# Kernel optimization log

Measured on AMD Instinct MI355X. Metric: run time of the kernel, lower is better.

Reference implementation:

```python
import jax, jax.numpy as jnp
import numpy as np

B, S, D, H, MEM, P = 32, 512, 768, 8, 768, 3
DK = D // H
LN_EPS = 1e-6


def _layer_norm(x, a, b):
    # torch LayerNorm in source uses unbiased std (ddof=1) and adds eps to std
    mean = x.mean(-1, keepdims=True)
    var = ((x - mean) ** 2).sum(-1, keepdims=True) / (x.shape[-1] - 1)
    return a * (x - mean) / (jnp.sqrt(var) + LN_EPS) + b


def _gcn_branch(x, mask, Wq, bq, Wk, bk, Ws, bs):
    # x: [B,S,D], mask: [B,S] 0/1 ints
    q = (x @ Wq.T + bq).reshape(B, S, H, DK).transpose(0, 2, 1, 3)  # [B,H,S,DK]
    k = (x @ Wk.T + bk).reshape(B, S, H, DK).transpose(0, 2, 1, 3)
    scores = jnp.einsum('bhqd,bhkd->bhqk', q, k) / jnp.sqrt(jnp.float32(DK))
    scores = jnp.where(mask[:, None, None, :] == 0, jnp.float32(-1e9), scores)
    adj = jax.nn.softmax(scores, axis=-1).mean(1)  # average heads -> [B,S,S]
    # adj - diag(diag(adj)) + I  ==  set diagonal to 1
    idx = jnp.arange(S)
    adj = adj.at[:, idx, idx].set(1.0)
    adj = adj * mask[:, :, None].astype(adj.dtype)  # src_mask.transpose(1,2) * adj
    denom = adj.sum(-1, keepdims=True) + 1.0
    out = x
    for W, b in zip(Ws, bs):
        out = jax.nn.relu((adj @ out @ W.T + b) / denom)
    return out, adj


def _proj(a, b):
    # Proj(a, b): (a.b / |b|) * normalize(b)
    b_mo = jnp.sqrt((b * b).sum(-1))
    axb = (a * b).sum(-1)
    bn = b / jnp.maximum(jnp.sqrt((b * b).sum(-1, keepdims=True)), 1e-12)
    return (axb / b_mo)[:, None] * bn


def setup_inputs() -> dict:
    key = jax.random.key(0)
    ks = jax.random.split(key, 32)

    def w(k, shape):
        return jax.random.normal(k, shape, jnp.float32) * 0.02

    inp = {
        'sequence_output': jax.random.normal(ks[0], (B, S, D), jnp.float32),
        'pooled_output': jax.random.normal(ks[1], (B, D), jnp.float32),
        'src_mask': jnp.ones((B, S), jnp.int32),
        'aspect_mask': jnp.ones((B, S), jnp.float32),
        'ln_a': jnp.ones((D,), jnp.float32),
        'ln_b': jnp.zeros((D,), jnp.float32),
        'fp_Wq': w(ks[2], (D, D)), 'fp_bq': jnp.zeros((D,), jnp.float32),
        'fp_Wk': w(ks[3], (D, D)), 'fp_bk': jnp.zeros((D,), jnp.float32),
        'fp_W0': w(ks[4], (MEM, D)), 'fp_b0': jnp.zeros((MEM,), jnp.float32),
        'fp_W1': w(ks[5], (MEM, MEM)), 'fp_b1': jnp.zeros((MEM,), jnp.float32),
        'fc_Wq': w(ks[6], (D, D)), 'fc_bq': jnp.zeros((D,), jnp.float32),
        'fc_Wk': w(ks[7], (D, D)), 'fc_bk': jnp.zeros((D,), jnp.float32),
        'fc_W0': w(ks[8], (MEM, D)), 'fc_b0': jnp.zeros((MEM,), jnp.float32),
        'fc_W1': w(ks[9], (MEM, MEM)), 'fc_b1': jnp.zeros((MEM,), jnp.float32),
        'fp_dense_W': w(ks[10], (P, MEM)), 'fp_dense_b': jnp.zeros((P,), jnp.float32),
        'fc_dense_W': w(ks[11], (P, MEM)), 'fc_dense_b': jnp.zeros((P,), jnp.float32),
    }
    return inp


def reference(sequence_output, pooled_output, src_mask, aspect_mask,
              ln_a, ln_b,
              fp_Wq, fp_bq, fp_Wk, fp_bk, fp_W0, fp_b0, fp_W1, fp_b1,
              fc_Wq, fc_bq, fc_Wk, fc_bk, fc_W0, fc_b0, fc_W1, fc_b1,
              fp_dense_W, fp_dense_b, fc_dense_W, fc_dense_b):
    label_embedding = pooled_output
    att_inputs = _layer_norm(sequence_output, ln_a, ln_b)  # dropout disabled (eval)
    asp_wn = aspect_mask.sum(1)[:, None]  # [B,1]

    fp_out, _ = _gcn_branch(att_inputs, src_mask, fp_Wq, fp_bq, fp_Wk, fp_bk,
                            [fp_W0, fp_W1], [fp_b0, fp_b1])
    fc_out, _ = _gcn_branch(att_inputs, src_mask, fc_Wq, fc_bq, fc_Wk, fc_bk,
                            [fc_W0, fc_W1], [fc_b0, fc_b1])

    outputs_fp = fp_out.sum(1)  # [B,MEM]
    outputs_fc = (fc_out * aspect_mask[:, :, None]).sum(1) / asp_wn  # [B,MEM]

    fp_x = _proj(outputs_fp, outputs_fc)
    fp_y = _proj(outputs_fp, outputs_fp - fp_x)
    fc_y = outputs_fc  # gradient-reverse layer is identity in forward

    logits_p = fp_y @ fp_dense_W.T + fp_dense_b
    logits_c = fc_y @ fc_dense_W.T + fc_dense_b
    return (logits_p, logits_c, fp_y, label_embedding)
```

## Files before the change

### kernel.cpp

```cpp
#include <hip/hip_runtime.h>
#include <math.h>
#include <stdint.h>

#define Bn 32
#define Sn 512
#define Dn 768
#define Hn 8
#define DKn 96
#define Pn 3

typedef __bf16 bf16_t;
typedef bf16_t bf16x8 __attribute__((ext_vector_type(8)));
typedef float f32x4 __attribute__((ext_vector_type(4)));

__device__ __forceinline__ bf16_t f2bf(float f) { return (bf16_t)f; }

__device__ __forceinline__ void gload16(const void* g, void* l) {
    __builtin_amdgcn_global_load_lds((const __attribute__((address_space(1))) void*)g,
                                     (__attribute__((address_space(3))) void*)l, 16, 0, 0);
}

__device__ __forceinline__ float brsum(float v, float* red) {
    int t = threadIdx.x;
    red[t] = v; __syncthreads();
    #pragma unroll
    for (int o = 128; o > 0; o >>= 1) {
        if (t < o) red[t] += red[t + o];
        __syncthreads();
    }
    float r = red[0]; __syncthreads();
    return r;
}

__global__ __launch_bounds__(256) void ln_kernel(const float* __restrict__ in,
                                                 const float* __restrict__ ga,
                                                 const float* __restrict__ gb,
                                                 bf16_t* __restrict__ out) {
    __shared__ float red[256];
    long row = blockIdx.x;
    const float* x = in + row * Dn;
    bf16_t* y = out + row * Dn;
    int t = threadIdx.x;
    float v0 = x[t], v1 = x[t + 256], v2 = x[t + 512];
    float mean = brsum(v0 + v1 + v2, red) / (float)Dn;
    float d0 = v0 - mean, d1 = v1 - mean, d2 = v2 - mean;
    float ss = brsum(d0 * d0 + d1 * d1 + d2 * d2, red);
    float inv = 1.0f / (sqrtf(ss / (float)(Dn - 1)) + 1e-6f);
    y[t]       = f2bf(ga[t]       * d0 * inv + gb[t]);
    y[t + 256] = f2bf(ga[t + 256] * d1 * inv + gb[t + 256]);
    y[t + 512] = f2bf(ga[t + 512] * d2 * inv + gb[t + 512]);
}

__global__ __launch_bounds__(256) void cvt8(const float* __restrict__ s0,
                                            const float* __restrict__ s1,
                                            const float* __restrict__ s2,
                                            const float* __restrict__ s3,
                                            const float* __restrict__ s4,
                                            const float* __restrict__ s5,
                                            const float* __restrict__ s6,
                                            const float* __restrict__ s7,
                                            bf16_t* __restrict__ dst) {
    int y = blockIdx.y;
    const float* s = (y == 0) ? s0 : (y == 1) ? s1 : (y == 2) ? s2 : (y == 3) ? s3
                   : (y == 4) ? s4 : (y == 5) ? s5 : (y == 6) ? s6 : s7;
    long i = (long)blockIdx.x * 1024 + threadIdx.x * 4;
    float4 v = *reinterpret_cast<const float4*>(s + i);
    bf16_t* d = dst + (long)y * Dn * Dn + i;
    d[0] = f2bf(v.x); d[1] = f2bf(v.y); d[2] = f2bf(v.z); d[3] = f2bf(v.w);
}

__global__ __launch_bounds__(256) void biascat_k(const float* __restrict__ s0,
                                                 const float* __restrict__ s1,
                                                 const float* __restrict__ s2,
                                                 const float* __restrict__ s3,
                                                 const float* __restrict__ s4,
                                                 const float* __restrict__ s5,
                                                 const float* __restrict__ s6,
                                                 const float* __restrict__ s7,
                                                 float* __restrict__ dst) {
    int y = blockIdx.x;
    const float* s = (y == 0) ? s0 : (y == 1) ? s1 : (y == 2) ? s2 : (y == 3) ? s3
                   : (y == 4) ? s4 : (y == 5) ? s5 : (y == 6) ? s6 : s7;
    for (int i = threadIdx.x; i < Dn; i += 256) dst[(long)y * Dn + i] = s[i];
}

__global__ void zero_kernel(float* p, int n) {
    int i = blockIdx.x * 256 + threadIdx.x;
    if (i < n) p[i] = 0.0f;
}

template <int EPI>
__global__ __launch_bounds__(512, 1) void gemm256(
    const bf16_t* __restrict__ Ag, const bf16_t* __restrict__ Bg,
    bf16_t* __restrict__ Cg, float* __restrict__ outv,
    int lda, int ldb, int ldc, int K,
    long sAhi, long sAlo, long sBhi, long sBlo, long sChi, long sClo,
    int lgZ,
    const float* __restrict__ bias, long bias_zs,
    const float* __restrict__ denom,
    const float* __restrict__ aspw) {
    __shared__ __align__(16) bf16_t lds[4][2][8192];

    unsigned gx = gridDim.x, gy = gridDim.y;
    unsigned nwg = gx * gy * gridDim.z;
    unsigned flat = (blockIdx.z * gy + blockIdx.y) * gx + blockIdx.x;
    unsigned q8 = nwg >> 3, r8 = nwg & 7;
    unsigned xcd = flat & 7, idx = flat >> 3;
    unsigned swz = (xcd < r8 ? xcd * (q8 + 1) : r8 * (q8 + 1) + (xcd - r8) * q8) + idx;
    unsigned bx = swz % gx;
    unsigned rest = swz / gx;
    unsigned by = rest % gy;
    unsigned zz = rest / gy;
    int zb = zz >> lgZ;
    int zg = zz & ((1 << lgZ) - 1);
    long zful = zz;

    const bf16_t* A = Ag + zb * sAhi + zg * sAlo;
    const bf16_t* B = Bg + zb * sBhi + zg * sBlo;

    int n0 = bx * 256, m0 = by * 256;
    int tid = threadIdx.x;
    int lane = tid & 63, w = tid >> 6;
    int wm = w >> 2, wn = w & 3;

    const int NT = K >> 5;

    int srow = lane & 15;
    int skc = (lane >> 4) * 8;
    const bf16_t* Asrc0 = A + (size_t)(m0 + (w * 2 + 0) * 16 + srow) * lda + skc;
    const bf16_t* Asrc1 = A + (size_t)(m0 + (w * 2 + 1) * 16 + srow) * lda + skc;
    const bf16_t* Bsrc0 = B + (size_t)(n0 + (w * 2 + 0) * 16 + srow) * ldb + skc;
    const bf16_t* Bsrc1 = B + (size_t)(n0 + (w * 2 + 1) * 16 + srow) * ldb + skc;
    int c0off = (w * 2 + 0) * 512 + lane * 8;
    int c1off = (w * 2 + 1) * 512 + lane * 8;

    f32x4 acc[8][4];
    #pragma unroll
    for (int i = 0; i < 8; ++i)
        #pragma unroll
        for (int j = 0; j < 4; ++j) acc[i][j] = (f32x4){0.f, 0.f, 0.f, 0.f};

    #pragma unroll
    for (int tt = 0; tt < 3; ++tt) {
        gload16(Asrc0 + tt * 32, &lds[tt][0][c0off]);
        gload16(Asrc1 + tt * 32, &lds[tt][0][c1off]);
        gload16(Bsrc0 + tt * 32, &lds[tt][1][c0off]);
        gload16(Bsrc1 + tt * 32, &lds[tt][1][c1off]);
    }
    asm volatile("s_waitcnt vmcnt(8)" ::: "memory");
    __builtin_amdgcn_s_barrier();

    int aoff = wm * 8 * 512 + lane * 8;
    int boff = wn * 4 * 512 + lane * 8;

    for (int t = 0; t < NT; ++t) {
        const bf16_t* bufA = &lds[t & 3][0][0];
        const bf16_t* bufB = &lds[t & 3][1][0];
        int tn = t + 3;
        bf16_t* dA = &lds[tn & 3][0][0];
        bf16_t* dB = &lds[tn & 3][1][0];
        bool st = tn < NT;

        bf16x8 a[4], b[4];
        #pragma unroll
        for (int i = 0; i < 4; ++i)
            a[i] = *(const bf16x8*)(bufA + aoff + i * 512);
        #pragma unroll
        for (int j = 0; j < 4; ++j)
            b[j] = *(const bf16x8*)(bufB + boff + j * 512);
        if (st) {
            gload16(Asrc0 + tn * 32, dA + c0off);
            gload16(Bsrc0 + tn * 32, dB + c0off);
        }
        __builtin_amdgcn_s_barrier();
        asm volatile("s_waitcnt lgkmcnt(0)" ::: "memory");
        __builtin_amdgcn_sched_barrier(0);
        __builtin_amdgcn_s_setprio(1);
        #pragma unroll
        for (int i = 0; i < 4; ++i)
            #pragma unroll
            for (int j = 0; j < 4; ++j)
                acc[i][j] = __builtin_amdgcn_mfma_f32_16x16x32_bf16(a[i], b[j], acc[i][j], 0, 0, 0);
        __builtin_amdgcn_s_setprio(0);
        __builtin_amdgcn_s_barrier();

        #pragma unroll
        for (int i = 0; i < 4; ++i)
            a[i] = *(const bf16x8*)(bufA + aoff + (4 + i) * 512);
        if (st) {
            gload16(Asrc1 + tn * 32, dA + c1off);
            gload16(Bsrc1 + tn * 32, dB + c1off);
        }
        __builtin_amdgcn_s_barrier();
        asm volatile("s_waitcnt lgkmcnt(0)" ::: "memory");
        __builtin_amdgcn_sched_barrier(0);
        __builtin_amdgcn_s_setprio(1);
        #pragma unroll
        for (int i = 0; i < 4; ++i)
            #pragma unroll
            for (int j = 0; j < 4; ++j)
                acc[4 + i][j] = __builtin_amdgcn_mfma_f32_16x16x32_bf16(a[i], b[j], acc[4 + i][j], 0, 0, 0);
        __builtin_amdgcn_s_setprio(0);
        if (t + 3 < NT)      asm volatile("s_waitcnt vmcnt(8)" ::: "memory");
        else if (t + 2 < NT) asm volatile("s_waitcnt vmcnt(4)" ::: "memory");
        else                 asm volatile("s_waitcnt vmcnt(0)" ::: "memory");
        __builtin_amdgcn_s_barrier();
    }

    int nb = n0 + wn * 64 + (lane & 15);
    int mbase = m0 + wm * 128 + (lane >> 4) * 4;
    const float* bz = bias ? bias + zb * bias_zs : nullptr;

    if (EPI == 0) {
        bf16_t* Cz = Cg + zb * sChi + zg * sClo;
        #pragma unroll
        for (int i = 0; i < 8; ++i) {
            #pragma unroll
            for (int r = 0; r < 4; ++r) {
                long m = mbase + i * 16 + r;
                bf16_t* crow = Cz + m * (long)ldc;
                #pragma unroll
                for (int j = 0; j < 4; ++j) {
                    int col = nb + j * 16;
                    float v = acc[i][j][r];
                    if (bz) v += bz[col];
                    crow[col] = f2bf(v);
                }
            }
        }
    } else if (EPI == 1) {
        bf16_t* Cz = Cg + zb * sChi + zg * sClo;
        const float* dz = denom + zful * Sn;
        #pragma unroll
        for (int i = 0; i < 8; ++i) {
            #pragma unroll
            for (int r = 0; r < 4; ++r) {
                int m = mbase + i * 16 + r;
                float dinv = 1.0f / dz[m];
                bf16_t* crow = Cz + (long)m * ldc;
                #pragma unroll
                for (int j = 0; j < 4; ++j) {
                    float v = fmaxf((acc[i][j][r] + bz[nb + j * 16]) * dinv, 0.0f);
                    crow[nb + j * 16] = f2bf(v);
                }
            }
        }
    } else {
        const float* dz = denom + zful * Sn;
        float csum[4] = {0.f, 0.f, 0.f, 0.f};
        #pragma unroll
        for (int i = 0; i < 8; ++i) {
            #pragma unroll
            for (int r = 0; r < 4; ++r) {
                int m = mbase + i * 16 + r;
                float dinv = 1.0f / dz[m];
                float wgt = (aspw && zb) ? aspw[(long)zg * Sn + m] : 1.0f;
                #pragma unroll
                for (int j = 0; j < 4; ++j) {
                    float v = fmaxf((acc[i][j][r] + bz[nb + j * 16]) * dinv, 0.0f);
                    csum[j] += v * wgt;
                }
            }
        }
        #pragma unroll
        for (int j = 0; j < 4; ++j) {
            float s = csum[j];
            s += __shfl_xor(s, 16);
            s += __shfl_xor(s, 32);
            if (lane < 16) atomicAdd(&outv[zful * Dn + nb + j * 16], s);
        }
    }
}

__global__ __launch_bounds__(256) void fused_adj(
    const bf16_t* __restrict__ QK, bf16_t* __restrict__ adjb,
    float* __restrict__ denomv, const int* __restrict__ mask) {
    __shared__ __align__(16) bf16_t Ks[2][128 * 104];
    __shared__ float red[4][16];

    int L = blockIdx.x;
    int swzi = (L & 7) * 128 + (L >> 3);
    int brc = swzi >> 9;
    int rem = swzi & 511;
    int b = rem >> 4;
    int q0 = (rem & 15) * 32;

    int tid = threadIdx.x;
    int lane = tid & 63, w = tid >> 6;
    int mt = w >> 1, nh = w & 1;
    int g = lane >> 4, c = lane & 15;

    const int LDQ = 3072;
    const bf16_t* Qrow  = QK + ((long)b * Sn + q0 + mt * 16 + c) * LDQ + brc * 1536;
    const bf16_t* Kbase = QK + (long)b * Sn * LDQ + brc * 1536 + Dn;

    const int* mrow = mask + (long)b * Sn;
    unsigned mbits = 0;
    #pragma unroll
    for (int t = 0; t < 4; ++t)
        #pragma unroll
        for (int nj = 0; nj < 4; ++nj)
            if (mrow[t * 128 + nh * 64 + nj * 16 + c] != 0) mbits |= 1u << (t * 4 + nj);

    int srow[6], scc[6];
    #pragma unroll
    for (int p = 0; p < 6; ++p) { int gr = tid + p * 256; srow[p] = gr / 12; scc[p] = gr % 12; }

    f32x4 adjacc[4][4];
    #pragma unroll
    for (int t = 0; t < 4; ++t)
        #pragma unroll
        for (int nj = 0; nj < 4; ++nj) adjacc[t][nj] = (f32x4){0.f, 0.f, 0.f, 0.f};

    f32x4 S[4][4];
    bf16x8 kr0[6], kr1[6], aq[3], aqn[3];
    const float sal = 0.102062072615966f;

    #pragma unroll
    for (int p = 0; p < 6; ++p)
        kr0[p] = *(const bf16x8*)(Kbase + (long)srow[p] * LDQ + scc[p] * 8);
    #pragma unroll
    for (int ks = 0; ks < 3; ++ks)
        aq[ks] = *(const bf16x8*)(Qrow + ks * 32 + g * 8);
    #pragma unroll
    for (int p = 0; p < 6; ++p)
        *(bf16x8*)(&Ks[0][srow[p] * 104 + scc[p] * 8]) = kr0[p];
    #pragma unroll
    for (int p = 0; p < 6; ++p)
        kr1[p] = *(const bf16x8*)(Kbase + (long)(128 + srow[p]) * LDQ + scc[p] * 8);
    __syncthreads();

    for (int h = 0; h < Hn; ++h) {
        #pragma unroll
        for (int t = 0; t < 4; ++t)
            #pragma unroll
            for (int nj = 0; nj < 4; ++nj) S[t][nj] = (f32x4){0.f, 0.f, 0.f, 0.f};

        float rs[4];
        #pragma unroll
        for (int t = 0; t < 4; ++t) {
            int it = h * 4 + t;
            if (it + 2 < 32) {
                int nt = it + 2;
                const bf16_t* kp = Kbase + (long)((nt & 3) * 128) * LDQ + (nt >> 2) * 96;
                if ((t & 1) == 0) {
                    #pragma unroll
                    for (int p = 0; p < 6; ++p)
                        kr0[p] = *(const bf16x8*)(kp + (long)srow[p] * LDQ + scc[p] * 8);
                } else {
                    #pragma unroll
                    for (int p = 0; p < 6; ++p)
                        kr1[p] = *(const bf16x8*)(kp + (long)srow[p] * LDQ + scc[p] * 8);
                }
            }
            if (t == 2 && h < 7) {
                #pragma unroll
                for (int ks = 0; ks < 3; ++ks)
                    aqn[ks] = *(const bf16x8*)(Qrow + (h + 1) * 96 + ks * 32 + g * 8);
            }
            #pragma unroll
            for (int nj = 0; nj < 4; ++nj) {
                #pragma unroll
                for (int ks = 0; ks < 3; ++ks) {
                    bf16x8 bk = *(const bf16x8*)(&Ks[t & 1][(nh * 64 + nj * 16 + c) * 104 + ks * 32 + g * 8]);
                    S[t][nj] = __builtin_amdgcn_mfma_f32_16x16x32_bf16(aq[ks], bk, S[t][nj], 0, 0, 0);
                }
            }
            if (t == 3) {
                rs[0] = rs[1] = rs[2] = rs[3] = 0.f;
                #pragma unroll
                for (int tt = 0; tt < 4; ++tt)
                    #pragma unroll
                    for (int nj = 0; nj < 4; ++nj) {
                        float mkf = ((mbits >> (tt * 4 + nj)) & 1u) ? 1.0f : 0.0f;
                        #pragma unroll
                        for (int ri = 0; ri < 4; ++ri) {
                            float e = mkf * __expf(S[tt][nj][ri] * sal);
                            S[tt][nj][ri] = e;
                            rs[ri] += e;
                        }
                    }
                #pragma unroll
                for (int ri = 0; ri < 4; ++ri) {
                    rs[ri] += __shfl_xor(rs[ri], 1);
                    rs[ri] += __shfl_xor(rs[ri], 2);
                    rs[ri] += __shfl_xor(rs[ri], 4);
                    rs[ri] += __shfl_xor(rs[ri], 8);
                }
                if (c == 0) {
                    #pragma unroll
                    for (int ri = 0; ri < 4; ++ri) red[w][g * 4 + ri] = rs[ri];
                }
            }
            if (it + 1 < 32) {
                if ((t & 1) == 0) {
                    #pragma unroll
                    for (int p = 0; p < 6; ++p)
                        *(bf16x8*)(&Ks[1][srow[p] * 104 + scc[p] * 8]) = kr1[p];
                } else {
                    #pragma unroll
                    for (int p = 0; p < 6; ++p)
                        *(bf16x8*)(&Ks[0][srow[p] * 104 + scc[p] * 8]) = kr0[p];
                }
            }
            __syncthreads();
            if (t == 3) {
                float inv[4];
                #pragma unroll
                for (int ri = 0; ri < 4; ++ri)
                    inv[ri] = 0.125f / (red[w][g * 4 + ri] + red[w ^ 1][g * 4 + ri]);
                #pragma unroll
                for (int tt = 0; tt < 4; ++tt)
                    #pragma unroll
                    for (int nj = 0; nj < 4; ++nj)
                        #pragma unroll
                        for (int ri = 0; ri < 4; ++ri)
                            adjacc[tt][nj][ri] += S[tt][nj][ri] * inv[ri];
                if (h < 7) {
                    #pragma unroll
                    for (int ks = 0; ks < 3; ++ks) aq[ks] = aqn[ks];
                }
            }
        }
    }

    float rm[4];
    #pragma unroll
    for (int ri = 0; ri < 4; ++ri)
        rm[ri] = (mrow[q0 + mt * 16 + g * 4 + ri] != 0) ? 1.0f : 0.0f;
    float rs2[4] = {0.f, 0.f, 0.f, 0.f};
    #pragma unroll
    for (int t = 0; t < 4; ++t)
        #pragma unroll
        for (int nj = 0; nj < 4; ++nj) {
            int n = t * 128 + nh * 64 + nj * 16 + c;
            #pragma unroll
            for (int ri = 0; ri < 4; ++ri) {
                float v = adjacc[t][nj][ri];
                int q = q0 + mt * 16 + g * 4 + ri;
                if (n == q) v = 1.0f;
                v *= rm[ri];
                adjacc[t][nj][ri] = v;
                rs2[ri] += v;
            }
        }
    #pragma unroll
    for (int ri = 0; ri < 4; ++ri) {
        rs2[ri] += __shfl_xor(rs2[ri], 1);
        rs2[ri] += __shfl_xor(rs2[ri], 2);
        rs2[ri] += __shfl_xor(rs2[ri], 4);
        rs2[ri] += __shfl_xor(rs2[ri], 8);
    }
    __syncthreads();
    if (c == 0) {
        #pragma unroll
        for (int ri = 0; ri < 4; ++ri) red[w][g * 4 + ri] = rs2[ri];
    }
    __syncthreads();
    long zful = (long)brc * Bn + b;
    if (nh == 0 && c == 0) {
        #pragma unroll
        for (int ri = 0; ri < 4; ++ri)
            denomv[zful * Sn + q0 + mt * 16 + g * 4 + ri] =
                red[w][g * 4 + ri] + red[w ^ 1][g * 4 + ri] + 1.0f;
    }
    bf16_t* stg = &Ks[0][0];
    #pragma unroll
    for (int t = 0; t < 4; ++t)
        #pragma unroll
        for (int nj = 0; nj < 4; ++nj) {
            int n = t * 128 + nh * 64 + nj * 16 + c;
            #pragma unroll
            for (int ri = 0; ri < 4; ++ri)
                stg[(mt * 16 + g * 4 + ri) * 520 + n] = f2bf(adjacc[t][nj][ri]);
        }
    __syncthreads();
    bf16_t* arow = adjb + (zful * Sn + q0) * Sn;
    #pragma unroll
    for (int p = 0; p < 8; ++p) {
        int gr = tid + p * 256;
        int row = gr >> 6, cc = gr & 63;
        *(bf16x8*)(arow + (long)row * Sn + cc * 8) = *(const bf16x8*)(stg + row * 520 + cc * 8);
    }
}

__global__ __launch_bounds__(256) void final_kernel(const float* __restrict__ ofp,
                                                    const float* __restrict__ ofc_raw,
                                                    const float* __restrict__ aspect,
                                                    const float* __restrict__ pooled,
                                                    const float* __restrict__ fpdW,
                                                    const float* __restrict__ fpdb,
                                                    const float* __restrict__ fcdW,
                                                    const float* __restrict__ fcdb,
                                                    float* __restrict__ out) {
    __shared__ float red[256];
    __shared__ float fp[Dn], fc[Dn], fy[Dn];
    int b = blockIdx.x, t = threadIdx.x;
    float awv = aspect[(long)b * Sn + t] + aspect[(long)b * Sn + t + 256];
    float asp_wn = brsum(awv, red);
    for (int i = t; i < Dn; i += 256) {
        fp[i] = ofp[(long)b * Dn + i];
        fc[i] = ofc_raw[(long)b * Dn + i] / asp_wn;
    }
    __syncthreads();
    float p0 = 0.0f, p1 = 0.0f;
    for (int i = t; i < Dn; i += 256) { p0 += fc[i] * fc[i]; p1 += fp[i] * fc[i]; }
    float dfc2 = brsum(p0, red);
    float dfpfc = brsum(p1, red);
    float bmo = sqrtf(dfc2);
    float coef = dfpfc / bmo;
    float bden = fmaxf(bmo, 1e-12f);
    float q0 = 0.0f, q1 = 0.0f;
    for (int i = t; i < Dn; i += 256) {
        float tv = fp[i] - coef * fc[i] / bden;
        fy[i] = tv;
        q0 += tv * tv;
        q1 += fp[i] * tv;
    }
    float dt2 = brsum(q0, red);
    float dfpt = brsum(q1, red);
    float tmo = sqrtf(dt2);
    float coef2 = dfpt / tmo;
    float tden = fmaxf(tmo, 1e-12f);
    for (int i = t; i < Dn; i += 256) fy[i] = coef2 * fy[i] / tden;
    __syncthreads();
    for (int i = t; i < Dn; i += 256) out[2 * Bn * Pn + (long)b * Dn + i] = fy[i];
    for (int i = t; i < Dn; i += 256)
        out[2 * Bn * Pn + Bn * Dn + (long)b * Dn + i] = pooled[(long)b * Dn + i];
    for (int j = 0; j < Pn; j++) {
        float lp = 0.0f, lc = 0.0f;
        for (int i = t; i < Dn; i += 256) {
            lp += fy[i] * fpdW[(long)j * Dn + i];
            lc += fc[i] * fcdW[(long)j * Dn + i];
        }
        float rp = brsum(lp, red);
        float rc = brsum(lc, red);
        if (t == 0) {
            out[(long)b * Pn + j] = rp + fpdb[j];
            out[Bn * Pn + (long)b * Pn + j] = rc + fcdb[j];
        }
    }
}

extern "C" void kernel_launch(void* const* d_in, const int* in_sizes, int n_in,
                              void* d_out, int out_size, void* d_ws, size_t ws_size,
                              hipStream_t stream) {
    const float* seq     = (const float*)d_in[0];
    const float* pooled  = (const float*)d_in[1];
    const int*   src_msk = (const int*)d_in[2];
    const float* aspect  = (const float*)d_in[3];
    const float* ln_a    = (const float*)d_in[4];
    const float* ln_b    = (const float*)d_in[5];
    float* out = (float*)d_out;

    const long NTD = (long)Bn * Sn * Dn;
    const long NSS = (long)Bn * Sn * Sn;
    const long DD  = (long)Dn * Dn;
    const long SD  = (long)Sn * Dn;

    char* w = (char*)d_ws;
    bf16_t* xbf   = (bf16_t*)w;
    bf16_t* QK    = xbf + NTD;
    bf16_t* H1    = QK;
    bf16_t* XT    = QK + 2 * NTD;
    bf16_t* adjb  = QK + 4 * NTD;
    float*  denom = (float*)(adjb + 2 * NSS);
    float*  ofp   = denom + 2L * Bn * Sn;
    float*  bcat  = ofp + 2L * Bn * Dn;
    bf16_t* Wb    = (bf16_t*)(bcat + 8 * Dn);

    ln_kernel<<<dim3(Bn * Sn), dim3(256), 0, stream>>>(seq, ln_a, ln_b, xbf);
    zero_kernel<<<dim3((2 * Bn * Dn + 255) / 256), dim3(256), 0, stream>>>(ofp, 2 * Bn * Dn);

    cvt8<<<dim3(576, 8), dim3(256), 0, stream>>>(
        (const float*)d_in[6], (const float*)d_in[8],
        (const float*)d_in[14], (const float*)d_in[16],
        (const float*)d_in[10], (const float*)d_in[18],
        (const float*)d_in[12], (const float*)d_in[20], Wb);
    biascat_k<<<dim3(8), dim3(256), 0, stream>>>(
        (const float*)d_in[7], (const float*)d_in[9],
        (const float*)d_in[15], (const float*)d_in[17],
        (const float*)d_in[11], (const float*)d_in[19],
        (const float*)d_in[13], (const float*)d_in[21], bcat);

    gemm256<0><<<dim3(12, 64, 1), dim3(512), 0, stream>>>(
        xbf, Wb, QK, nullptr, Dn, Dn, 3072, Dn,
        0, 0, 0, 0, 0, 0, 0, bcat, 0, nullptr, nullptr);

    fused_adj<<<dim3(2 * Bn * Sn / 32), dim3(256), 0, stream>>>(QK, adjb, denom, src_msk);

    gemm256<0><<<dim3(2, 3, 64), dim3(512), 0, stream>>>(
        Wb + 4 * DD, xbf, XT, nullptr, Dn, Dn, Sn, Dn,
        DD, 0, 0, SD, 32 * SD, SD,
        5, nullptr, 0, nullptr, nullptr);

    gemm256<1><<<dim3(3, 2, 64), dim3(512), 0, stream>>>(
        adjb, XT, H1, nullptr, Sn, Sn, Dn, Sn,
        32L * Sn * Sn, (long)Sn * Sn, 32 * SD, SD, 32 * SD, SD,
        5, bcat + 4 * Dn, Dn, denom, nullptr);

    gemm256<0><<<dim3(2, 3, 64), dim3(512), 0, stream>>>(
        Wb + 6 * DD, H1, XT, nullptr, Dn, Dn, Sn, Dn,
        DD, 0, 32 * SD, SD, 32 * SD, SD,
        5, nullptr, 0, nullptr, nullptr);

    gemm256<2><<<dim3(3, 2, 64), dim3(512), 0, stream>>>(
        adjb, XT, nullptr, ofp, Sn, Sn, 0, Sn,
        32L * Sn * Sn, (long)Sn * Sn, 32 * SD, SD, 0, 0,
        5, bcat + 6 * Dn, Dn, denom, aspect);

    final_kernel<<<dim3(Bn), dim3(256), 0, stream>>>(
        ofp, ofp + (long)Bn * Dn, aspect, pooled,
        (const float*)d_in[22], (const float*)d_in[23],
        (const float*)d_in[24], (const float*)d_in[25], out);
}
```

Measured before the change: 513.9 us.

## Add simple 128x128 GEMM for batched GCN stages and drop LDS staging in fused_adj

Adds a new 128x128-tile, 256-thread GEMM kernel (single-buffered LDS, direct global-to-LDS loads) and uses it for the four batched GCN GEMMs in place of the 256x256 tile kernel. This gives more workgroups and more occupancy, at the cost of less data reuse per tile and no software pipelining. fused_adj now reads K fragments straight from global memory into registers, double-buffered in registers, instead of staging them through shared memory. This removes most of its barriers, and it now declares 2 blocks per CU. The 256x256 kernel keeps only its EPI 0 path, which the QK projection still uses.

```diff
diff --git a/kernel.cpp b/kernel.cpp
--- a/kernel.cpp
+++ b/kernel.cpp
@@ -90,16 +90,17 @@
 }
 
 template <int EPI>
-__global__ __launch_bounds__(512, 1) void gemm256(
+__global__ __launch_bounds__(256) void gemm_bt(
     const bf16_t* __restrict__ Ag, const bf16_t* __restrict__ Bg,
     bf16_t* __restrict__ Cg, float* __restrict__ outv,
     int lda, int ldb, int ldc, int K,
     long sAhi, long sAlo, long sBhi, long sBlo, long sChi, long sClo,
-    int lgZ,
+    int lgZ, float alpha,
     const float* __restrict__ bias, long bias_zs,
     const float* __restrict__ denom,
     const float* __restrict__ aspw) {
-    __shared__ __align__(16) bf16_t lds[4][2][8192];
+    __shared__ __align__(16) bf16_t As[128 * 32];
+    __shared__ __align__(16) bf16_t Bs[128 * 32];
 
     unsigned gx = gridDim.x, gy = gridDim.y;
     unsigned nwg = gx * gy * gridDim.z;
@@ -118,6 +119,145 @@
     const bf16_t* A = Ag + zb * sAhi + zg * sAlo;
     const bf16_t* B = Bg + zb * sBhi + zg * sBlo;
 
+    int n0 = bx * 128;
+    int m0 = by * 128;
+    int tid = threadIdx.x;
+    int lane = tid & 63, wv = tid >> 6;
+    int wm = wv >> 1, wn = wv & 1;
+
+    int sub = lane >> 2;
+    int kcol = (lane & 3) * 8;
+    const bf16_t* pA0 = A + (size_t)(m0 + wv * 16 + sub) * lda + kcol;
+    const bf16_t* pA1 = pA0 + (size_t)64 * lda;
+    const bf16_t* pB0 = B + (size_t)(n0 + wv * 16 + sub) * ldb + kcol;
+    const bf16_t* pB1 = pB0 + (size_t)64 * ldb;
+    bf16_t* lA0 = As + wv * 512 + lane * 8;
+    bf16_t* lA1 = As + (4 + wv) * 512 + lane * 8;
+    bf16_t* lB0 = Bs + wv * 512 + lane * 8;
+    bf16_t* lB1 = Bs + (4 + wv) * 512 + lane * 8;
+
+    f32x4 acc[4][4];
+    #pragma unroll
+    for (int i = 0; i < 4; i++)
+        #pragma unroll
+        for (int j = 0; j < 4; j++) acc[i][j] = (f32x4){0.f, 0.f, 0.f, 0.f};
+
+    const bf16_t* ar = As + (wm * 64 + (lane & 15)) * 32 + (lane >> 4) * 8;
+    const bf16_t* br = Bs + (wn * 64 + (lane & 15)) * 32 + (lane >> 4) * 8;
+
+    for (int k0 = 0; k0 < K; k0 += 32) {
+        gload16(pA0 + k0, lA0);
+        gload16(pA1 + k0, lA1);
+        gload16(pB0 + k0, lB0);
+        gload16(pB1 + k0, lB1);
+        __syncthreads();
+        bf16x8 a[4], b[4];
+        #pragma unroll
+        for (int i = 0; i < 4; i++) a[i] = *(const bf16x8*)(ar + i * 16 * 32);
+        #pragma unroll
+        for (int j = 0; j < 4; j++) b[j] = *(const bf16x8*)(br + j * 16 * 32);
+        #pragma unroll
+        for (int i = 0; i < 4; i++)
+            #pragma unroll
+            for (int j = 0; j < 4; j++)
+                acc[i][j] = __builtin_amdgcn_mfma_f32_16x16x32_bf16(a[i], b[j], acc[i][j], 0, 0, 0);
+        __syncthreads();
+    }
+
+    int nb = n0 + wn * 64 + (lane & 15);
+    int mbase = m0 + wm * 64 + (lane >> 4) * 4;
+    const float* bz = bias ? bias + zb * bias_zs : nullptr;
+
+    if (EPI == 0) {
+        bf16_t* Cz = Cg + zb * sChi + zg * sClo;
+        #pragma unroll
+        for (int i = 0; i < 4; i++) {
+            #pragma unroll
+            for (int r = 0; r < 4; r++) {
+                long m = mbase + i * 16 + r;
+                bf16_t* crow = Cz + m * (long)ldc;
+                #pragma unroll
+                for (int j = 0; j < 4; j++) {
+                    int col = nb + j * 16;
+                    float v = acc[i][j][r] * alpha;
+                    if (bz) v += bz[col];
+                    crow[col] = f2bf(v);
+                }
+            }
+        }
+    } else if (EPI == 1) {
+        bf16_t* Cz = Cg + zb * sChi + zg * sClo;
+        const float* dz = denom + zful * Sn;
+        #pragma unroll
+        for (int i = 0; i < 4; i++) {
+            #pragma unroll
+            for (int r = 0; r < 4; r++) {
+                int m = mbase + i * 16 + r;
+                float dinv = 1.0f / dz[m];
+                bf16_t* crow = Cz + (long)m * ldc;
+                #pragma unroll
+                for (int j = 0; j < 4; j++) {
+                    float v = fmaxf((acc[i][j][r] + bz[nb + j * 16]) * dinv, 0.0f);
+                    crow[nb + j * 16] = f2bf(v);
+                }
+            }
+        }
+    } else {
+        const float* dz = denom + zful * Sn;
+        float csum[4] = {0.f, 0.f, 0.f, 0.f};
+        #pragma unroll
+        for (int i = 0; i < 4; i++) {
+            #pragma unroll
+            for (int r = 0; r < 4; r++) {
+                int m = mbase + i * 16 + r;
+                float dinv = 1.0f / dz[m];
+                float wgt = (aspw && zb) ? aspw[(long)zg * Sn + m] : 1.0f;
+                #pragma unroll
+                for (int j = 0; j < 4; j++) {
+                    float v = fmaxf((acc[i][j][r] + bz[nb + j * 16]) * dinv, 0.0f);
+                    csum[j] += v * wgt;
+                }
+            }
+        }
+        #pragma unroll
+        for (int j = 0; j < 4; j++) {
+            float s = csum[j];
+            s += __shfl_xor(s, 16);
+            s += __shfl_xor(s, 32);
+            if (lane < 16) atomicAdd(&outv[zful * Dn + nb + j * 16], s);
+        }
+    }
+}
+
+template <int EPI>
+__global__ __launch_bounds__(512, 1) void gemm256(
+    const bf16_t* __restrict__ Ag, const bf16_t* __restrict__ Bg,
+    bf16_t* __restrict__ Cg, float* __restrict__ outv,
+    int lda, int ldb, int ldc, int K,
+    long sAhi, long sAlo, long sBhi, long sBlo, long sChi, long sClo,
+    int lgZ,
+    const float* __restrict__ bias, long bias_zs,
+    const float* __restrict__ denom,
+    const float* __restrict__ aspw) {
+    __shared__ __align__(16) bf16_t lds[4][2][8192];
+
+    unsigned gx = gridDim.x, gy = gridDim.y;
+    unsigned nwg = gx * gy * gridDim.z;
+    unsigned flat = (blockIdx.z * gy + blockIdx.y) * gx + blockIdx.x;
+    unsigned q8 = nwg >> 3, r8 = nwg & 7;
+    unsigned xcd = flat & 7, idx = flat >> 3;
+    unsigned swz = (xcd < r8 ? xcd * (q8 + 1) : r8 * (q8 + 1) + (xcd - r8) * q8) + idx;
+    unsigned bx = swz % gx;
+    unsigned rest = swz / gx;
+    unsigned by = rest % gy;
+    unsigned zz = rest / gy;
+    int zb = zz >> lgZ;
+    int zg = zz & ((1 << lgZ) - 1);
+    long zful = zz;
+
+    const bf16_t* A = Ag + zb * sAhi + zg * sAlo;
+    const bf16_t* B = Bg + zb * sBhi + zg * sBlo;
+
     int n0 = bx * 256, m0 = by * 256;
     int tid = threadIdx.x;
     int lane = tid & 63, w = tid >> 6;
@@ -228,54 +368,13 @@
                 }
             }
         }
-    } else if (EPI == 1) {
-        bf16_t* Cz = Cg + zb * sChi + zg * sClo;
-        const float* dz = denom + zful * Sn;
-        #pragma unroll
-        for (int i = 0; i < 8; ++i) {
-            #pragma unroll
-            for (int r = 0; r < 4; ++r) {
-                int m = mbase + i * 16 + r;
-                float dinv = 1.0f / dz[m];
-                bf16_t* crow = Cz + (long)m * ldc;
-                #pragma unroll
-                for (int j = 0; j < 4; ++j) {
-                    float v = fmaxf((acc[i][j][r] + bz[nb + j * 16]) * dinv, 0.0f);
-                    crow[nb + j * 16] = f2bf(v);
-                }
-            }
-        }
-    } else {
-        const float* dz = denom + zful * Sn;
-        float csum[4] = {0.f, 0.f, 0.f, 0.f};
-        #pragma unroll
-        for (int i = 0; i < 8; ++i) {
-            #pragma unroll
-            for (int r = 0; r < 4; ++r) {
-                int m = mbase + i * 16 + r;
-                float dinv = 1.0f / dz[m];
-                float wgt = (aspw && zb) ? aspw[(long)zg * Sn + m] : 1.0f;
-                #pragma unroll
-                for (int j = 0; j < 4; ++j) {
-                    float v = fmaxf((acc[i][j][r] + bz[nb + j * 16]) * dinv, 0.0f);
-                    csum[j] += v * wgt;
-                }
-            }
-        }
-        #pragma unroll
-        for (int j = 0; j < 4; ++j) {
-            float s = csum[j];
-            s += __shfl_xor(s, 16);
-            s += __shfl_xor(s, 32);
-            if (lane < 16) atomicAdd(&outv[zful * Dn + nb + j * 16], s);
-        }
-    }
-}
-
-__global__ __launch_bounds__(256) void fused_adj(
+    }
+}
+
+__global__ __launch_bounds__(256, 2) void fused_adj(
     const bf16_t* __restrict__ QK, bf16_t* __restrict__ adjb,
     float* __restrict__ denomv, const int* __restrict__ mask) {
-    __shared__ __align__(16) bf16_t Ks[2][128 * 104];
+    __shared__ __align__(16) bf16_t stg[32 * 520];
     __shared__ float red[4][16];
 
     int L = blockIdx.x;
@@ -290,9 +389,9 @@
     int mt = w >> 1, nh = w & 1;
     int g = lane >> 4, c = lane & 15;
 
-    const int LDQ = 3072;
-    const bf16_t* Qrow  = QK + ((long)b * Sn + q0 + mt * 16 + c) * LDQ + brc * 1536;
-    const bf16_t* Kbase = QK + (long)b * Sn * LDQ + brc * 1536 + Dn;
+    const long LDQ = 3072;
+    const bf16_t* Qrow = QK + ((long)b * Sn + q0 + mt * 16 + c) * LDQ + brc * 1536 + g * 8;
+    const bf16_t* Kbase = QK + ((long)b * Sn + nh * 64 + c) * LDQ + brc * 1536 + Dn + g * 8;
 
     const int* mrow = mask + (long)b * Sn;
     unsigned mbits = 0;
@@ -302,125 +401,113 @@
         for (int nj = 0; nj < 4; ++nj)
             if (mrow[t * 128 + nh * 64 + nj * 16 + c] != 0) mbits |= 1u << (t * 4 + nj);
 
-    int srow[6], scc[6];
-    #pragma unroll
-    for (int p = 0; p < 6; ++p) { int gr = tid + p * 256; srow[p] = gr / 12; scc[p] = gr % 12; }
-
     f32x4 adjacc[4][4];
     #pragma unroll
     for (int t = 0; t < 4; ++t)
         #pragma unroll
         for (int nj = 0; nj < 4; ++nj) adjacc[t][nj] = (f32x4){0.f, 0.f, 0.f, 0.f};
 
-    f32x4 S[4][4];
-    bf16x8 kr0[6], kr1[6], aq[3], aqn[3];
+    bf16x8 krA[6], krB[6], aq[3], aqn[3];
     const float sal = 0.102062072615966f;
 
     #pragma unroll
-    for (int p = 0; p < 6; ++p)
-        kr0[p] = *(const bf16x8*)(Kbase + (long)srow[p] * LDQ + scc[p] * 8);
+    for (int jj = 0; jj < 2; ++jj)
+        #pragma unroll
+        for (int ks = 0; ks < 3; ++ks)
+            krA[jj * 3 + ks] = *(const bf16x8*)(Kbase + (long)(jj * 16) * LDQ + ks * 32);
     #pragma unroll
     for (int ks = 0; ks < 3; ++ks)
-        aq[ks] = *(const bf16x8*)(Qrow + ks * 32 + g * 8);
-    #pragma unroll
-    for (int p = 0; p < 6; ++p)
-        *(bf16x8*)(&Ks[0][srow[p] * 104 + scc[p] * 8]) = kr0[p];
-    #pragma unroll
-    for (int p = 0; p < 6; ++p)
-        kr1[p] = *(const bf16x8*)(Kbase + (long)(128 + srow[p]) * LDQ + scc[p] * 8);
-    __syncthreads();
+        aq[ks] = *(const bf16x8*)(Qrow + ks * 32);
 
     for (int h = 0; h < Hn; ++h) {
+        f32x4 S[4][4];
         #pragma unroll
         for (int t = 0; t < 4; ++t)
             #pragma unroll
             for (int nj = 0; nj < 4; ++nj) S[t][nj] = (f32x4){0.f, 0.f, 0.f, 0.f};
 
-        float rs[4];
-        #pragma unroll
-        for (int t = 0; t < 4; ++t) {
-            int it = h * 4 + t;
-            if (it + 2 < 32) {
-                int nt = it + 2;
-                const bf16_t* kp = Kbase + (long)((nt & 3) * 128) * LDQ + (nt >> 2) * 96;
-                if ((t & 1) == 0) {
+        #pragma unroll
+        for (int ht = 0; ht < 8; ++ht) {
+            const int t = ht >> 1, half = ht & 1;
+            const int nht = (ht + 1) & 7;
+            const int hinc = (ht == 7) ? 1 : 0;
+            const int t2 = nht >> 1, half2 = nht & 1;
+            const bf16_t* kb2 = Kbase + (long)(t2 * 128) * LDQ + (long)(h + hinc) * 96;
+            if ((ht & 1) == 0) {
+                #pragma unroll
+                for (int jj = 0; jj < 2; ++jj)
                     #pragma unroll
-                    for (int p = 0; p < 6; ++p)
-                        kr0[p] = *(const bf16x8*)(kp + (long)srow[p] * LDQ + scc[p] * 8);
-                } else {
+                    for (int ks = 0; ks < 3; ++ks)
+                        krB[jj * 3 + ks] = *(const bf16x8*)(kb2 + (long)((half2 * 2 + jj) * 16) * LDQ + ks * 32);
+            } else {
+                #pragma unroll
+                for (int jj = 0; jj < 2; ++jj)
                     #pragma unroll
-                    for (int p = 0; p < 6; ++p)
-                        kr1[p] = *(const bf16x8*)(kp + (long)srow[p] * LDQ + scc[p] * 8);
+                    for (int ks = 0; ks < 3; ++ks)
+                        krA[jj * 3 + ks] = *(const bf16x8*)(kb2 + (long)((half2 * 2 + jj) * 16) * LDQ + ks * 32);
+            }
+            if (ht == 6) {
+                #pragma unroll
+                for (int ks = 0; ks < 3; ++ks)
+                    aqn[ks] = *(const bf16x8*)(Qrow + (long)(h + 1) * 96 + ks * 32);
+            }
+            if ((ht & 1) == 0) {
+                #pragma unroll
+                for (int jj = 0; jj < 2; ++jj)
+                    #pragma unroll
+                    for (int ks = 0; ks < 3; ++ks)
+                        S[t][half * 2 + jj] = __builtin_amdgcn_mfma_f32_16x16x32_bf16(
+                            aq[ks], krA[jj * 3 + ks], S[t][half * 2 + jj], 0, 0, 0);
+            } else {
+                #pragma unroll
+                for (int jj = 0; jj < 2; ++jj)
+                    #pragma unroll
+                    for (int ks = 0; ks < 3; ++ks)
+                        S[t][half * 2 + jj] = __builtin_amdgcn_mfma_f32_16x16x32_bf16(
+                            aq[ks], krB[jj * 3 + ks], S[t][half * 2 + jj], 0, 0, 0);
+            }
+        }
+
+        float rs[4] = {0.f, 0.f, 0.f, 0.f};
+        #pragma unroll
+        for (int t = 0; t < 4; ++t)
+            #pragma unroll
+            for (int nj = 0; nj < 4; ++nj) {
+                float mkf = ((mbits >> (t * 4 + nj)) & 1u) ? 1.0f : 0.0f;
+                #pragma unroll
+                for (int ri = 0; ri < 4; ++ri) {
+                    float e = mkf * __expf(S[t][nj][ri] * sal);
+                    S[t][nj][ri] = e;
+                    rs[ri] += e;
                 }
             }
-            if (t == 2 && h < 7) {
-                #pragma unroll
-                for (int ks = 0; ks < 3; ++ks)
-                    aqn[ks] = *(const bf16x8*)(Qrow + (h + 1) * 96 + ks * 32 + g * 8);
-            }
-            #pragma unroll
-            for (int nj = 0; nj < 4; ++nj) {
-                #pragma unroll
-                for (int ks = 0; ks < 3; ++ks) {
-                    bf16x8 bk = *(const bf16x8*)(&Ks[t & 1][(nh * 64 + nj * 16 + c) * 104 + ks * 32 + g * 8]);
-                    S[t][nj] = __builtin_amdgcn_mfma_f32_16x16x32_bf16(aq[ks], bk, S[t][nj], 0, 0, 0);
-                }
-            }
-            if (t == 3) {
-                rs[0] = rs[1] = rs[2] = rs[3] = 0.f;
-                #pragma unroll
-                for (int tt = 0; tt < 4; ++tt)
-                    #pragma unroll
-                    for (int nj = 0; nj < 4; ++nj) {
-                        float mkf = ((mbits >> (tt * 4 + nj)) & 1u) ? 1.0f : 0.0f;
-                        #pragma unroll
-                        for (int ri = 0; ri < 4; ++ri) {
-                            float e = mkf * __expf(S[tt][nj][ri] * sal);
-                            S[tt][nj][ri] = e;
-                            rs[ri] += e;
-                        }
-                    }
-                #pragma unroll
-                for (int ri = 0; ri < 4; ++ri) {
-                    rs[ri] += __shfl_xor(rs[ri], 1);
-                    rs[ri] += __shfl_xor(rs[ri], 2);
-                    rs[ri] += __shfl_xor(rs[ri], 4);
-                    rs[ri] += __shfl_xor(rs[ri], 8);
-                }
-                if (c == 0) {
-                    #pragma unroll
-                    for (int ri = 0; ri < 4; ++ri) red[w][g * 4 + ri] = rs[ri];
-                }
-            }
-            if (it + 1 < 32) {
-                if ((t & 1) == 0) {
-                    #pragma unroll
-                    for (int p = 0; p < 6; ++p)
-                        *(bf16x8*)(&Ks[1][srow[p] * 104 + scc[p] * 8]) = kr1[p];
-                } else {
-                    #pragma unroll
-                    for (int p = 0; p < 6; ++p)
-                        *(bf16x8*)(&Ks[0][srow[p] * 104 + scc[p] * 8]) = kr0[p];
-                }
-            }
-            __syncthreads();
-            if (t == 3) {
-                float inv[4];
+        #pragma unroll
+        for (int ri = 0; ri < 4; ++ri) {
+            rs[ri] += __shfl_xor(rs[ri], 1);
+            rs[ri] += __shfl_xor(rs[ri], 2);
+            rs[ri] += __shfl_xor(rs[ri], 4);
+            rs[ri] += __shfl_xor(rs[ri], 8);
+        }
+        if (c == 0) {
+            #pragma unroll
+            for (int ri = 0; ri < 4; ++ri) red[w][g * 4 + ri] = rs[ri];
+        }
+        __syncthreads();
+        float inv[4];
+        #pragma unroll
+        for (int ri = 0; ri < 4; ++ri)
+            inv[ri] = 0.125f / (red[w][g * 4 + ri] + red[w ^ 1][g * 4 + ri]);
+        __syncthreads();
+        #pragma unroll
+        for (int t = 0; t < 4; ++t)
+            #pragma unroll
+            for (int nj = 0; nj < 4; ++nj)
                 #pragma unroll
                 for (int ri = 0; ri < 4; ++ri)
-                    inv[ri] = 0.125f / (red[w][g * 4 + ri] + red[w ^ 1][g * 4 + ri]);
-                #pragma unroll
-                for (int tt = 0; tt < 4; ++tt)
-                    #pragma unroll
-                    for (int nj = 0; nj < 4; ++nj)
-                        #pragma unroll
-                        for (int ri = 0; ri < 4; ++ri)
-                            adjacc[tt][nj][ri] += S[tt][nj][ri] * inv[ri];
-                if (h < 7) {
-                    #pragma unroll
-                    for (int ks = 0; ks < 3; ++ks) aq[ks] = aqn[ks];
-                }
-            }
+                    adjacc[t][nj][ri] += S[t][nj][ri] * inv[ri];
+        if (h < 7) {
+            #pragma unroll
+            for (int ks = 0; ks < 3; ++ks) aq[ks] = aqn[ks];
         }
     }
 
@@ -451,7 +538,6 @@
         rs2[ri] += __shfl_xor(rs2[ri], 4);
         rs2[ri] += __shfl_xor(rs2[ri], 8);
     }
-    __syncthreads();
     if (c == 0) {
         #pragma unroll
         for (int ri = 0; ri < 4; ++ri) red[w][g * 4 + ri] = rs2[ri];
@@ -464,7 +550,6 @@
             denomv[zful * Sn + q0 + mt * 16 + g * 4 + ri] =
                 red[w][g * 4 + ri] + red[w ^ 1][g * 4 + ri] + 1.0f;
     }
-    bf16_t* stg = &Ks[0][0];
     #pragma unroll
     for (int t = 0; t < 4; ++t)
         #pragma unroll
@@ -589,25 +674,25 @@
 
     fused_adj<<<dim3(2 * Bn * Sn / 32), dim3(256), 0, stream>>>(QK, adjb, denom, src_msk);
 
-    gemm256<0><<<dim3(2, 3, 64), dim3(512), 0, stream>>>(
+    gemm_bt<0><<<dim3(4, 6, 64), dim3(256), 0, stream>>>(
         Wb + 4 * DD, xbf, XT, nullptr, Dn, Dn, Sn, Dn,
         DD, 0, 0, SD, 32 * SD, SD,
-        5, nullptr, 0, nullptr, nullptr);
-
-    gemm256<1><<<dim3(3, 2, 64), dim3(512), 0, stream>>>(
+        5, 1.0f, nullptr, 0, nullptr, nullptr);
+
+    gemm_bt<1><<<dim3(6, 4, 64), dim3(256), 0, stream>>>(
         adjb, XT, H1, nullptr, Sn, Sn, Dn, Sn,
         32L * Sn * Sn, (long)Sn * Sn, 32 * SD, SD, 32 * SD, SD,
-        5, bcat + 4 * Dn, Dn, denom, nullptr);
-
-    gemm256<0><<<dim3(2, 3, 64), dim3(512), 0, stream>>>(
+        5, 1.0f, bcat + 4 * Dn, Dn, denom, nullptr);
+
+    gemm_bt<0><<<dim3(4, 6, 64), dim3(256), 0, stream>>>(
         Wb + 6 * DD, H1, XT, nullptr, Dn, Dn, Sn, Dn,
         DD, 0, 32 * SD, SD, 32 * SD, SD,
-        5, nullptr, 0, nullptr, nullptr);
-
-    gemm256<2><<<dim3(3, 2, 64), dim3(512), 0, stream>>>(
+        5, 1.0f, nullptr, 0, nullptr, nullptr);
+
+    gemm_bt<2><<<dim3(6, 4, 64), dim3(256), 0, stream>>>(
         adjb, XT, nullptr, ofp, Sn, Sn, 0, Sn,
         32L * Sn * Sn, (long)Sn * Sn, 32 * SD, SD, 0, 0,
-        5, bcat + 6 * Dn, Dn, denom, aspect);
+        5, 1.0f, bcat + 6 * Dn, Dn, denom, aspect);
 
     final_kernel<<<dim3(Bn), dim3(256), 0, stream>>>(
         ofp, ofp + (long)Bn * Dn, aspect, pooled,
```

Result: slower. 566.4 us (+10.2%).
